# Kernel optimization log

Measured on AMD Instinct MI355X. Metric: run time of the kernel, lower is better.

## Reference

```python
import jax, jax.numpy as jnp
import numpy as np

H = 512
NHALF = 32  # N // 2 complex conjugate pairs
LLEN = 8192


def setup_inputs() -> dict:
    key = jax.random.key(0)
    k1, k2, k3 = jax.random.split(key, 3)
    # log_dt ~ uniform in [log(dt_min), log(dt_max)]
    log_dt = jax.random.uniform(k1, (H,), dtype=jnp.float32) * (
        np.log(0.1) - np.log(0.001)) + np.log(0.001)
    # C: complex randn stored as (H, NHALF, 2) real view
    C = jax.random.normal(k2, (H, NHALF, 2), dtype=jnp.float32)
    log_A_real = jnp.log(0.5 * jnp.ones((H, NHALF), dtype=jnp.float32))
    A_imag = np.pi * jnp.broadcast_to(
        jnp.arange(NHALF, dtype=jnp.float32), (H, NHALF))
    return {"C": C, "log_dt": log_dt, "log_A_real": log_A_real,
            "A_imag": A_imag, "L": LLEN}


def reference(C, log_dt, log_A_real, A_imag, L):
    # zoh discretization of diagonal SSM -> kernel K of shape (H, L)
    dt = jnp.exp(log_dt)                                  # (H,)
    Cc = (C[..., 0] + 1j * C[..., 1]).astype(jnp.complex64)  # (H, n)
    A = (-jnp.exp(log_A_real) + 1j * A_imag).astype(jnp.complex64)  # (H, n)
    dtA = A * dt[:, None]                                 # (H, n)
    t = jnp.arange(L, dtype=jnp.float32)                  # (L,)
    C_scaled = Cc * (jnp.exp(dtA) - 1.0) / A              # (H, n)
    # Vandermonde: exp(dtA)^t over length L, reduce over n
    T = jnp.exp(dtA[:, :, None] * t[None, None, :])       # (H, n, L) complex
    K = 2.0 * jnp.einsum('hn,hnl->hl', C_scaled, T).real  # (H, L)
    return K
```

## Files before the change

### kernel.cpp

```cpp
#include <hip/hip_runtime.h>
#include <math.h>

#define HDIM   512
#define NH     32
#define NP     16
#define LLEN   8192
#define BLOCK  256
#define LSPLIT 2
#define LPB    (LLEN / LSPLIT)
#define LPT    16

typedef float vf2 __attribute__((ext_vector_type(2)));
#define VFMA(a, b, c) __builtin_elementwise_fma((a), (b), (c))

__global__ __launch_bounds__(BLOCK) void s4d_kernel(
    const float* __restrict__ C,
    const float* __restrict__ log_dt,
    const float* __restrict__ log_A_real,
    const float* __restrict__ A_imag,
    float* __restrict__ out)
{
    __shared__ float4 tabA[NP][16];
    __shared__ float4 tabB[NP][16];
    __shared__ float4 s_w [NP];
    __shared__ float4 s_pq[NP];
    __shared__ float4 s_p2[NP];

    const int h   = blockIdx.y;
    const int ls  = blockIdx.x;
    const int tid = threadIdx.x;

    {
        const int n = tid & 31;
        const int g = tid >> 5;
        const int P = n >> 1, o = n & 1;
        const double dt  = exp((double)log_dt[h]);
        const double Are = -exp((double)log_A_real[h * NH + n]);
        const double Aim = (double)A_imag[h * NH + n];
        const double dre = Are * dt, dim = Aim * dt;

        double s1, c1; sincos(dim, &s1, &c1);
        const double em  = exp(dre);
        const double w1r = em * c1, w1i = em * s1;

        float* tabAf = (float*)&tabA[0][0];
        float* tabBf = (float*)&tabB[0][0];

        if (g < 4) {
            const double nre = w1r - 1.0, nim = w1i;
            const double den = Are * Are + Aim * Aim;
            const double fre = (nre * Are + nim * Aim) / den;
            const double fim = (nim * Are - nre * Aim) / den;
            const double Cre = (double)C[(h * NH + n) * 2 + 0];
            const double Cim = (double)C[(h * NH + n) * 2 + 1];
            const double csr = 2.0 * (Cre * fre - Cim * fim);
            const double csi = 2.0 * (Cre * fim + Cim * fre);

            const int    i0   = g * 4;
            const double base = 16.0 * (double)i0;
            double s0, c0; sincos(dim * base, &s0, &c0);
            const double m0 = exp(dre * base);
            const double er = m0 * c0, ei = m0 * s0;
            double gr = csr * er - csi * ei;
            double gi = csr * ei + csi * er;
            double ss, cs; sincos(dim * 16.0, &ss, &cs);
            const double ms  = exp(dre * 16.0);
            const double str = ms * cs, sti = ms * ss;
            for (int k = 0; k < 4; ++k) {
                const int idx = (P * 16 + i0 + k) * 4;
                tabAf[idx + o]     = (float)gr;
                tabAf[idx + 2 + o] = (float)gi;
                const double t = gr * str - gi * sti;
                gi = gr * sti + gi * str;
                gr = t;
            }
        } else {
            const int    i0   = (g - 4) * 4;
            const double base = (double)(LPB * ls) + 256.0 * (double)i0;
            double s0, c0; sincos(dim * base, &s0, &c0);
            const double m0 = exp(dre * base);
            double er = m0 * c0, ei = m0 * s0;
            double ss, cs; sincos(dim * 256.0, &ss, &cs);
            const double ms  = exp(dre * 256.0);
            const double str = ms * cs, sti = ms * ss;
            for (int k = 0; k < 4; ++k) {
                const int idx = (P * 16 + i0 + k) * 4;
                tabBf[idx + o]     = (float)er;
                tabBf[idx + 2 + o] = (float)ei;
                const double t = er * str - ei * sti;
                ei = er * sti + ei * str;
                er = t;
            }
        }

        if (g == 0) {
            float* wf  = (float*)&s_w[0];
            float* pqf = (float*)&s_pq[0];
            float* p2f = (float*)&s_p2[0];
            const double p  = 2.0 * w1r;
            const double q  = em * em;
            const double p2 = 2.0 * (w1r * w1r - w1i * w1i);
            const double q2 = q * q;
            wf [P * 4 + o]     = (float)w1r;
            wf [P * 4 + 2 + o] = (float)w1i;
            pqf[P * 4 + o]     = (float)p;
            pqf[P * 4 + 2 + o] = (float)q;
            p2f[P * 4 + o]     = (float)p2;
            p2f[P * 4 + 2 + o] = (float)q2;
        }
    }
    __syncthreads();

    const int lo = tid & 15, hi = tid >> 4;

    vf2 acc[LPT];
#pragma unroll
    for (int l = 0; l < LPT; ++l) acc[l] = (vf2)(0.f);

#pragma unroll 2
    for (int P = 0; P < NP; ++P) {
        const float4 a4  = tabA[P][lo];
        const float4 b4  = tabB[P][hi];
        const float4 w4  = s_w[P];
        const float4 pq4 = s_pq[P];
        const float4 p24 = s_p2[P];

        const vf2 Ax = {a4.x, a4.y}, Ay = {a4.z, a4.w};
        const vf2 Bx = {b4.x, b4.y}, By = {b4.z, b4.w};
        const vf2 wr = {w4.x, w4.y}, wi = {w4.z, w4.w};
        const vf2 p  = {pq4.x, pq4.y}, q  = {pq4.z, pq4.w};
        const vf2 p2 = {p24.x, p24.y}, q2 = {p24.z, p24.w};

        const vf2 Tr = VFMA(Ax, Bx, -(Ay * By));
        const vf2 Ti = VFMA(Ax, By,  (Ay * Bx));
        const vf2 y0 = Tr;
        const vf2 y1 = VFMA(Tr, wr, -(Ti * wi));
        const vf2 y2 = VFMA(p, y1, -(q * y0));
        const vf2 y3 = VFMA(p, y2, -(q * y1));
        acc[0] += y0; acc[1] += y1; acc[2] += y2; acc[3] += y3;

        vf2 e0 = y0, e1 = y2, o0 = y1, o1 = y3;
#pragma unroll
        for (int m = 0; m < 6; ++m) {
            const vf2 e2 = VFMA(p2, e1, -(q2 * e0));
            const vf2 o2 = VFMA(p2, o1, -(q2 * o0));
            acc[4 + 2 * m] += e2;
            acc[5 + 2 * m] += o2;
            e0 = e1; e1 = e2;
            o0 = o1; o1 = o2;
        }
    }

    float* orow = out + (size_t)h * LLEN + ls * LPB + LPT * tid;
#pragma unroll
    for (int j = 0; j < 4; ++j) {
        *(float4*)(orow + 4 * j) = make_float4(
            acc[4*j+0].x + acc[4*j+0].y,
            acc[4*j+1].x + acc[4*j+1].y,
            acc[4*j+2].x + acc[4*j+2].y,
            acc[4*j+3].x + acc[4*j+3].y);
    }
}

extern "C" void kernel_launch(void* const* d_in, const int* in_sizes, int n_in,
                              void* d_out, int out_size, void* d_ws, size_t ws_size,
                              hipStream_t stream) {
    const float* C          = (const float*)d_in[0];
    const float* log_dt     = (const float*)d_in[1];
    const float* log_A_real = (const float*)d_in[2];
    const float* A_imag     = (const float*)d_in[3];
    float* out = (float*)d_out;

    dim3 grid(LSPLIT, HDIM);
    s4d_kernel<<<grid, BLOCK, 0, stream>>>(C, log_dt, log_A_real, A_imag, out);
}
```

Measured before the change: 81.12 us.

## Split table precompute into separate prep kernel and prefetch tables from global

Moves the double-precision table and recurrence-coefficient computation out of the main kernel into a separate prep kernel that writes to workspace. The main kernel reads the tables from global memory with one-iteration-ahead prefetch instead of building them in LDS behind a barrier. Arithmetic is expressed as explicit packed-FP32 inline asm. This removes the duplicated per-block fp64 transcendental work and the barrier, at the cost of an extra launch, global traffic for the tables, and asm that limits compiler scheduling.

```diff
diff --git a/kernel.cpp b/kernel.cpp
--- a/kernel.cpp
+++ b/kernel.cpp
@@ -11,144 +11,147 @@
 #define LPT    16
 
 typedef float vf2 __attribute__((ext_vector_type(2)));
-#define VFMA(a, b, c) __builtin_elementwise_fma((a), (b), (c))
 
-__global__ __launch_bounds__(BLOCK) void s4d_kernel(
-    const float* __restrict__ C,
-    const float* __restrict__ log_dt,
-    const float* __restrict__ log_A_real,
-    const float* __restrict__ A_imag,
-    float* __restrict__ out)
+static __device__ inline vf2 pk_mul(vf2 a, vf2 b) {
+    vf2 d; asm("v_pk_mul_f32 %0, %1, %2" : "=v"(d) : "v"(a), "v"(b)); return d;
+}
+static __device__ inline vf2 pk_add(vf2 a, vf2 b) {
+    vf2 d; asm("v_pk_add_f32 %0, %1, %2" : "=v"(d) : "v"(a), "v"(b)); return d;
+}
+static __device__ inline vf2 pk_fma(vf2 a, vf2 b, vf2 c) {
+    vf2 d; asm("v_pk_fma_f32 %0, %1, %2, %3" : "=v"(d) : "v"(a), "v"(b), "v"(c)); return d;
+}
+static __device__ inline vf2 pk_fms(vf2 a, vf2 b, vf2 c) {
+    vf2 d; asm("v_pk_fma_f32 %0, %1, %2, %3 neg_lo:[0,0,1] neg_hi:[0,0,1]"
+               : "=v"(d) : "v"(a), "v"(b), "v"(c)); return d;
+}
+
+#define TABA_F4  (HDIM * NP * 16)
+#define TABB_F4  (HDIM * 2 * NP * 16)
+#define PAD_F4   64
+#define TABB_OFF (TABA_F4 + PAD_F4)
+#define CST_OFF  (TABB_OFF + TABB_F4 + PAD_F4)
+
+__global__ __launch_bounds__(64) void s4d_prep(
+    const float* __restrict__ C, const float* __restrict__ log_dt,
+    const float* __restrict__ log_A_real, const float* __restrict__ A_imag,
+    float* __restrict__ ws)
 {
-    __shared__ float4 tabA[NP][16];
-    __shared__ float4 tabB[NP][16];
-    __shared__ float4 s_w [NP];
-    __shared__ float4 s_pq[NP];
-    __shared__ float4 s_p2[NP];
+    const int idx = blockIdx.x * 64 + threadIdx.x;
+    const int h = idx >> 5, n = idx & 31;
+    const int P = n >> 1,  o = n & 1;
 
-    const int h   = blockIdx.y;
-    const int ls  = blockIdx.x;
-    const int tid = threadIdx.x;
+    const double dt  = exp((double)log_dt[h]);
+    const double Are = -exp((double)log_A_real[h * NH + n]);
+    const double Aim = (double)A_imag[h * NH + n];
+    const double dre = Are * dt, dim = Aim * dt;
+
+    double s1, c1; sincos(dim, &s1, &c1);
+    const double em  = exp(dre);
+    const double w1r = em * c1, w1i = em * s1;
+
+    const double nre = w1r - 1.0, nim = w1i;
+    const double den = Are * Are + Aim * Aim;
+    const double fre = (nre * Are + nim * Aim) / den;
+    const double fim = (nim * Are - nre * Aim) / den;
+    const double Cre = (double)C[(h * NH + n) * 2 + 0];
+    const double Cim = (double)C[(h * NH + n) * 2 + 1];
+    const double csr = 2.0 * (Cre * fre - Cim * fim);
+    const double csi = 2.0 * (Cre * fim + Cim * fre);
 
     {
-        const int n = tid & 31;
-        const int g = tid >> 5;
-        const int P = n >> 1, o = n & 1;
-        const double dt  = exp((double)log_dt[h]);
-        const double Are = -exp((double)log_A_real[h * NH + n]);
-        const double Aim = (double)A_imag[h * NH + n];
-        const double dre = Are * dt, dim = Aim * dt;
+        const double p  = 2.0 * w1r, q = em * em;
+        const double p2 = 2.0 * (w1r * w1r - w1i * w1i), q2 = q * q;
+        float* cc = ws + (size_t)CST_OFF * 4 + (size_t)(h * NP + P) * 12;
+        cc[0 + o]  = (float)w1r;  cc[2 + o]  = (float)w1i;
+        cc[4 + o]  = (float)p;    cc[6 + o]  = (float)q;
+        cc[8 + o]  = (float)p2;   cc[10 + o] = (float)q2;
+    }
 
-        double s1, c1; sincos(dim, &s1, &c1);
-        const double em  = exp(dre);
-        const double w1r = em * c1, w1i = em * s1;
+    {
+        double ss, cs; sincos(dim * 16.0, &ss, &cs);
+        const double ms = exp(dre * 16.0);
+        const double str = ms * cs, sti = ms * ss;
+        double gr = csr, gi = csi;
+        float* ta = ws + (size_t)(h * NP + P) * 16 * 4;
+        for (int lo = 0; lo < 16; ++lo) {
+            ta[lo * 4 + o]     = (float)gr;
+            ta[lo * 4 + 2 + o] = (float)gi;
+            const double t = gr * str - gi * sti;
+            gi = gr * sti + gi * str; gr = t;
+        }
+    }
 
-        float* tabAf = (float*)&tabA[0][0];
-        float* tabBf = (float*)&tabB[0][0];
-
-        if (g < 4) {
-            const double nre = w1r - 1.0, nim = w1i;
-            const double den = Are * Are + Aim * Aim;
-            const double fre = (nre * Are + nim * Aim) / den;
-            const double fim = (nim * Are - nre * Aim) / den;
-            const double Cre = (double)C[(h * NH + n) * 2 + 0];
-            const double Cim = (double)C[(h * NH + n) * 2 + 1];
-            const double csr = 2.0 * (Cre * fre - Cim * fim);
-            const double csi = 2.0 * (Cre * fim + Cim * fre);
-
-            const int    i0   = g * 4;
-            const double base = 16.0 * (double)i0;
-            double s0, c0; sincos(dim * base, &s0, &c0);
-            const double m0 = exp(dre * base);
-            const double er = m0 * c0, ei = m0 * s0;
-            double gr = csr * er - csi * ei;
-            double gi = csr * ei + csi * er;
-            double ss, cs; sincos(dim * 16.0, &ss, &cs);
-            const double ms  = exp(dre * 16.0);
-            const double str = ms * cs, sti = ms * ss;
-            for (int k = 0; k < 4; ++k) {
-                const int idx = (P * 16 + i0 + k) * 4;
-                tabAf[idx + o]     = (float)gr;
-                tabAf[idx + 2 + o] = (float)gi;
-                const double t = gr * str - gi * sti;
-                gi = gr * sti + gi * str;
-                gr = t;
-            }
-        } else {
-            const int    i0   = (g - 4) * 4;
-            const double base = (double)(LPB * ls) + 256.0 * (double)i0;
-            double s0, c0; sincos(dim * base, &s0, &c0);
-            const double m0 = exp(dre * base);
-            double er = m0 * c0, ei = m0 * s0;
-            double ss, cs; sincos(dim * 256.0, &ss, &cs);
-            const double ms  = exp(dre * 256.0);
-            const double str = ms * cs, sti = ms * ss;
-            for (int k = 0; k < 4; ++k) {
-                const int idx = (P * 16 + i0 + k) * 4;
-                tabBf[idx + o]     = (float)er;
-                tabBf[idx + 2 + o] = (float)ei;
+    {
+        double ss, cs; sincos(dim * 256.0, &ss, &cs);
+        const double ms = exp(dre * 256.0);
+        const double str = ms * cs, sti = ms * ss;
+        double er = 1.0, ei = 0.0;
+        for (int ls = 0; ls < 2; ++ls) {
+            float* tb = ws + (size_t)TABB_OFF * 4
+                           + (size_t)(((h * 2 + ls) * NP + P) * 16) * 4;
+            for (int hi = 0; hi < 16; ++hi) {
+                tb[hi * 4 + o]     = (float)er;
+                tb[hi * 4 + 2 + o] = (float)ei;
                 const double t = er * str - ei * sti;
-                ei = er * sti + ei * str;
-                er = t;
+                ei = er * sti + ei * str; er = t;
             }
         }
+    }
+}
 
-        if (g == 0) {
-            float* wf  = (float*)&s_w[0];
-            float* pqf = (float*)&s_pq[0];
-            float* p2f = (float*)&s_p2[0];
-            const double p  = 2.0 * w1r;
-            const double q  = em * em;
-            const double p2 = 2.0 * (w1r * w1r - w1i * w1i);
-            const double q2 = q * q;
-            wf [P * 4 + o]     = (float)w1r;
-            wf [P * 4 + 2 + o] = (float)w1i;
-            pqf[P * 4 + o]     = (float)p;
-            pqf[P * 4 + 2 + o] = (float)q;
-            p2f[P * 4 + o]     = (float)p2;
-            p2f[P * 4 + 2 + o] = (float)q2;
-        }
-    }
-    __syncthreads();
+__global__ __launch_bounds__(BLOCK) void s4d_main(
+    const float4* __restrict__ ws4, float* __restrict__ out)
+{
+    const int h  = blockIdx.y, ls = blockIdx.x, tid = threadIdx.x;
+    const int lo = tid & 15,  hi = tid >> 4;
 
-    const int lo = tid & 15, hi = tid >> 4;
+    const float4* pa = ws4 + (size_t)(h * NP) * 16 + lo;
+    const float4* pb = ws4 + TABB_OFF + (size_t)((h * 2 + ls) * NP) * 16 + hi;
+    const float4* pc = ws4 + CST_OFF + (size_t)(h * NP) * 3;
 
     vf2 acc[LPT];
 #pragma unroll
     for (int l = 0; l < LPT; ++l) acc[l] = (vf2)(0.f);
 
-#pragma unroll 2
+    float4 a4 = pa[0], b4 = pb[0];
+
+#pragma unroll 1
     for (int P = 0; P < NP; ++P) {
-        const float4 a4  = tabA[P][lo];
-        const float4 b4  = tabB[P][hi];
-        const float4 w4  = s_w[P];
-        const float4 pq4 = s_pq[P];
-        const float4 p24 = s_p2[P];
+        const float4 na = pa[(P + 1) * 16];
+        const float4 nb = pb[(P + 1) * 16];
+        const float4 c0 = pc[P * 3 + 0];
+        const float4 c1 = pc[P * 3 + 1];
+        const float4 c2 = pc[P * 3 + 2];
 
         const vf2 Ax = {a4.x, a4.y}, Ay = {a4.z, a4.w};
         const vf2 Bx = {b4.x, b4.y}, By = {b4.z, b4.w};
-        const vf2 wr = {w4.x, w4.y}, wi = {w4.z, w4.w};
-        const vf2 p  = {pq4.x, pq4.y}, q  = {pq4.z, pq4.w};
-        const vf2 p2 = {p24.x, p24.y}, q2 = {p24.z, p24.w};
+        const vf2 wr = {c0.x, c0.y}, wi = {c0.z, c0.w};
+        const vf2 p  = {c1.x, c1.y}, q  = {c1.z, c1.w};
+        const vf2 p2 = {c2.x, c2.y}, q2 = {c2.z, c2.w};
 
-        const vf2 Tr = VFMA(Ax, Bx, -(Ay * By));
-        const vf2 Ti = VFMA(Ax, By,  (Ay * Bx));
+        const vf2 Tr = pk_fms(Ax, Bx, pk_mul(Ay, By));
+        const vf2 Ti = pk_fma(Ax, By, pk_mul(Ay, Bx));
         const vf2 y0 = Tr;
-        const vf2 y1 = VFMA(Tr, wr, -(Ti * wi));
-        const vf2 y2 = VFMA(p, y1, -(q * y0));
-        const vf2 y3 = VFMA(p, y2, -(q * y1));
-        acc[0] += y0; acc[1] += y1; acc[2] += y2; acc[3] += y3;
+        const vf2 y1 = pk_fms(Tr, wr, pk_mul(Ti, wi));
+        const vf2 y2 = pk_fms(p, y1, pk_mul(q, y0));
+        const vf2 y3 = pk_fms(p, y2, pk_mul(q, y1));
+        acc[0] = pk_add(acc[0], y0);
+        acc[1] = pk_add(acc[1], y1);
+        acc[2] = pk_add(acc[2], y2);
+        acc[3] = pk_add(acc[3], y3);
 
         vf2 e0 = y0, e1 = y2, o0 = y1, o1 = y3;
 #pragma unroll
         for (int m = 0; m < 6; ++m) {
-            const vf2 e2 = VFMA(p2, e1, -(q2 * e0));
-            const vf2 o2 = VFMA(p2, o1, -(q2 * o0));
-            acc[4 + 2 * m] += e2;
-            acc[5 + 2 * m] += o2;
+            const vf2 e2 = pk_fms(p2, e1, pk_mul(q2, e0));
+            const vf2 o2 = pk_fms(p2, o1, pk_mul(q2, o0));
+            acc[4 + 2 * m] = pk_add(acc[4 + 2 * m], e2);
+            acc[5 + 2 * m] = pk_add(acc[5 + 2 * m], o2);
             e0 = e1; e1 = e2;
             o0 = o1; o1 = o2;
         }
+        a4 = na; b4 = nb;
     }
 
     float* orow = out + (size_t)h * LLEN + ls * LPB + LPT * tid;
@@ -170,7 +173,9 @@
     const float* log_A_real = (const float*)d_in[2];
     const float* A_imag     = (const float*)d_in[3];
     float* out = (float*)d_out;
+    float* ws  = (float*)d_ws;
 
+    s4d_prep<<<HDIM * NH / 64, 64, 0, stream>>>(C, log_dt, log_A_real, A_imag, ws);
     dim3 grid(LSPLIT, HDIM);
-    s4d_kernel<<<grid, BLOCK, 0, stream>>>(C, log_dt, log_A_real, A_imag, out);
+    s4d_main<<<grid, BLOCK, 0, stream>>>((const float4*)ws, out);
 }
```

New measurement: 86.81 us. 1.07x slower.
